# Kernel tuning notes

Hardware: AMD Instinct MI355X
Metric: run time of the kernel (lower is better)

Reference implementation:

```python
import jax, jax.numpy as jnp
import numpy as np

FM = 80            # feature_maps
N_ROUNDS = 32
NORM_EPS = 1e-3
LOSS_EPS = 1e-8


def _relu6(x):
    return jnp.clip(x, 0.0, 6.0)


def _norm(x):
    # tf.nn.moments over axis 0 + batch_normalization (no scale/offset)
    mean = jnp.mean(x, axis=0, keepdims=True)
    var = jnp.var(x, axis=0, keepdims=True)
    return (x - mean) * jax.lax.rsqrt(var + NORM_EPS)


def setup_inputs() -> dict:
    key = jax.random.key(0)
    n_vars, n_clauses, n_graphs, lits_per_clause = 100000, 420000, 100, 3
    n_cells = n_clauses * lits_per_clause
    ks = jax.random.split(key, 24)

    lit_var = jax.random.randint(ks[0], (n_cells,), 0, n_vars, dtype=jnp.int32)
    lit_neg = jax.random.randint(ks[1], (n_cells,), 0, 2, dtype=jnp.int32)
    clause_idx = jnp.repeat(jnp.arange(n_clauses, dtype=jnp.int32), lits_per_clause)
    clause_graph = jnp.repeat(jnp.arange(n_graphs, dtype=jnp.int32), n_clauses // n_graphs)

    def dense(k, fi, fo):
        return jax.random.normal(k, (fi, fo), jnp.float32) / np.sqrt(fi)

    inp = dict(
        lit_var=lit_var, lit_neg=lit_neg, clause_idx=clause_idx, clause_graph=clause_graph,
        n_vars=n_vars, n_clauses=n_clauses, n_graphs=n_graphs,
        L_init_scale=jnp.float32(1.0 / np.sqrt(FM)),
        C_init_scale=jnp.float32(1.0 / np.sqrt(FM)),
        LC_scale=jnp.float32(0.1), CL_scale=jnp.float32(0.1),
        # L_update MLP: in=3*FM (L, CL_msgs, flip(L)) -> hidden 3*FM relu6 -> FM
        Lu_W0=dense(ks[2], 3 * FM, 3 * FM), Lu_b0=jnp.zeros((3 * FM,), jnp.float32),
        Lu_W1=dense(ks[3], 3 * FM, FM),     Lu_b1=jnp.zeros((FM,), jnp.float32),
        # C_update MLP: in=2*FM (C, LC_msgs) -> hidden 2*FM relu6 -> FM
        Cu_W0=dense(ks[4], 2 * FM, 2 * FM), Cu_b0=jnp.zeros((2 * FM,), jnp.float32),
        Cu_W1=dense(ks[5], 2 * FM, FM),     Cu_b1=jnp.zeros((FM,), jnp.float32),
        # V_score MLP: in=2*FM -> 3 hidden relu6 layers of 2*FM -> 1
        Vs_W0=dense(ks[6], 2 * FM, 2 * FM), Vs_b0=jnp.zeros((2 * FM,), jnp.float32),
        Vs_W1=dense(ks[7], 2 * FM, 2 * FM), Vs_b1=jnp.zeros((2 * FM,), jnp.float32),
        Vs_W2=dense(ks[8], 2 * FM, 2 * FM), Vs_b2=jnp.zeros((2 * FM,), jnp.float32),
        Vs_W3=dense(ks[9], 2 * FM, 1),      Vs_b3=jnp.zeros((1,), jnp.float32),
    )
    return inp


def reference(lit_var, lit_neg, clause_idx, clause_graph, n_vars, n_clauses, n_graphs,
              L_init_scale, C_init_scale, LC_scale, CL_scale,
              Lu_W0, Lu_b0, Lu_W1, Lu_b1,
              Cu_W0, Cu_b0, Cu_W1, Cu_b1,
              Vs_W0, Vs_b0, Vs_W1, Vs_b1, Vs_W2, Vs_b2, Vs_W3, Vs_b3):
    n_lits = 2 * n_vars
    lit_row = lit_var + lit_neg * n_vars          # row in L for each cell
    sign = (1 - 2 * lit_neg).astype(jnp.float32)  # +1 positive literal, -1 negated

    def mlp_L(x):
        return _relu6(x @ Lu_W0 + Lu_b0) @ Lu_W1 + Lu_b1

    def mlp_C(x):
        return _relu6(x @ Cu_W0 + Cu_b0) @ Cu_W1 + Cu_b1

    def v_score(x):
        h = _relu6(x @ Vs_W0 + Vs_b0)
        h = _relu6(h @ Vs_W1 + Vs_b1)
        h = _relu6(h @ Vs_W2 + Vs_b2)
        return h @ Vs_W3 + Vs_b3

    def flip(L):
        return jnp.concatenate([L[n_vars:], L[:n_vars]], axis=0)

    def per_round_loss(logits):
        # softplus_mixed_loss over ragged clauses of signed literals
        lit_vals = logits[lit_var, 0] * sign                         # [n_cells]
        clause_sum = jax.ops.segment_sum(jax.nn.softplus(lit_vals), clause_idx,
                                         num_segments=n_clauses)     # [n_clauses]
        vc = jnp.exp(-clause_sum)
        per_clause = vc * (-jnp.log(1.0 - vc + LOSS_EPS))
        per_graph = jax.ops.segment_sum(per_clause, clause_graph, num_segments=n_graphs)
        return jnp.sum(jnp.sqrt(per_graph + 1e-6))

    L0 = jnp.ones((n_lits, FM), jnp.float32) * L_init_scale
    C0 = jnp.ones((n_clauses, FM), jnp.float32) * C_init_scale

    def round_fn(carry, _):
        L, C, loss = carry
        # CL^T @ L  (sparse gather + segment-sum over clause cells)
        LC_msgs = jax.ops.segment_sum(L[lit_row], clause_idx, num_segments=n_clauses) * LC_scale
        C = _norm(mlp_C(jnp.concatenate([C, LC_msgs], axis=-1)))
        # adj @ C  (scatter-add clause features back to literal rows)
        CL_msgs = jax.ops.segment_sum(C[clause_idx], lit_row, num_segments=n_lits) * CL_scale
        L = _norm(mlp_L(jnp.concatenate([L, CL_msgs, flip(L)], axis=-1)))
        V = jnp.concatenate([L[:n_vars], L[n_vars:]], axis=1)        # [n_vars, 2*FM]
        logits = v_score(V)
        loss = loss + per_round_loss(logits)
        return (L, C, loss), None

    (L, C, loss), _ = jax.lax.scan(round_fn, (L0, C0, jnp.float32(0.0)), None, length=N_ROUNDS)
    # final-round logits (recomputed from the final L state, identical math)
    logits = v_score(jnp.concatenate([L[:n_vars], L[n_vars:]], axis=1))
    return logits, loss / N_ROUNDS
```

## Files before the change

kernel.cpp:

```cpp
#include <hip/hip_runtime.h>
#include <hip/hip_fp8.h>
#include <math.h>


#define NROUNDS 32
#define NORM_EPS 1e-3f
#define LOSS_EPS 1e-8f

static constexpr int NV_CONST = 100000;
static constexpr int NG_CONST = 100;

typedef __attribute__((ext_vector_type(8))) short short8;
typedef __attribute__((ext_vector_type(8))) unsigned char uchar8;
typedef __attribute__((ext_vector_type(16))) unsigned char uchar16;
typedef __attribute__((ext_vector_type(4))) float f32x4;

__device__ __forceinline__ short f2bf(float f) {
    union { float f; unsigned u; } x; x.f = f;
    unsigned r = x.u + 0x7fffu + ((x.u >> 16) & 1u);
    return (short)(r >> 16);
}
__device__ __forceinline__ float bf2f(short s) {
    union { unsigned u; float f; } x; x.u = ((unsigned)(unsigned short)s) << 16;
    return x.f;
}
__device__ __forceinline__ unsigned char f2q8(float f) {
    f = fminf(fmaxf(f, -448.f), 448.f);
    __hip_fp8_e4m3 t(f);
    return t.__x;
}
__device__ __forceinline__ float q82f(unsigned char b) {
    __hip_fp8_e4m3 t; t.__x = b;
    return (float)t;
}


__global__ void k_zero_i(int* __restrict__ p, int n) {
    int i = blockIdx.x * 256 + threadIdx.x;
    if (i < n) p[i] = 0;
}
__global__ void k_fill_b(short* __restrict__ p, int n, const float* __restrict__ vp) {
    int i = blockIdx.x * 256 + threadIdx.x;
    if (i < n) p[i] = f2bf(*vp);
}
__global__ void k_fill_q8(unsigned char* __restrict__ p, int n, const float* __restrict__ vp) {
    int i = blockIdx.x * 256 + threadIdx.x;
    if (i < n) p[i] = f2q8(*vp);
}
__global__ void k_copy_int(int* __restrict__ dst, const int* __restrict__ src, int n) {
    int i = blockIdx.x * 256 + threadIdx.x;
    if (i < n) dst[i] = src[i];
}
__global__ void k_init_slabs(float* __restrict__ slabC, float* __restrict__ slabL,
                             float* __restrict__ loss_a, float nclf) {
    int i = blockIdx.x * 256 + threadIdx.x;
    if (i < 33 * 160) {
        slabC[i] = (i >= 80 && i < 160) ? nclf * (1.f - NORM_EPS) : 0.f;
        slabL[i] = 0.f;
    }
    if (i == 0) loss_a[0] = 0.f;
}

__global__ void k_litrow(const int* __restrict__ lit_var, const int* __restrict__ lit_neg,
                         int* __restrict__ litrow, int* __restrict__ lofs4,
                         int* __restrict__ counts, int ncell, int nv) {
    int i = blockIdx.x * 256 + threadIdx.x;
    if (i < ncell) {
        int r = lit_var[i] + lit_neg[i] * nv;
        litrow[i] = r;
        int cl = i / 3, t = i - cl * 3;
        lofs4[cl * 4 + t] = r * 8;
        atomicAdd(&counts[r], 1);
    }
}

__launch_bounds__(1024)
__global__ void k_scan4(const int* __restrict__ counts, int* __restrict__ row_ptr,
                        int n, int total) {
    __shared__ int sd[1024];
    __shared__ int carry;
    int tid = threadIdx.x;
    if (tid == 0) carry = 0;
    __syncthreads();
    for (int base = 0; base < n; base += 4096) {
        int i0 = base + tid * 4;
        int a0 = (i0 + 0 < n) ? counts[i0 + 0] : 0;
        int a1 = (i0 + 1 < n) ? counts[i0 + 1] : 0;
        int a2 = (i0 + 2 < n) ? counts[i0 + 2] : 0;
        int a3 = (i0 + 3 < n) ? counts[i0 + 3] : 0;
        int s = a0 + a1 + a2 + a3;
        sd[tid] = s;
        __syncthreads();
        for (int off = 1; off < 1024; off <<= 1) {
            int t = (tid >= off) ? sd[tid - off] : 0;
            __syncthreads();
            sd[tid] += t;
            __syncthreads();
        }
        int excl = carry + sd[tid] - s;
        if (i0 + 0 < n) row_ptr[i0 + 0] = excl;
        if (i0 + 1 < n) row_ptr[i0 + 1] = excl + a0;
        if (i0 + 2 < n) row_ptr[i0 + 2] = excl + a0 + a1;
        if (i0 + 3 < n) row_ptr[i0 + 3] = excl + a0 + a1 + a2;
        __syncthreads();
        if (tid == 0) carry += sd[1023];
        __syncthreads();
    }
    if (tid == 0) row_ptr[n] = total;
}

__global__ void k_fill_csr(const int* __restrict__ litrow, const int* __restrict__ clause_idx,
                           int* __restrict__ cursor, int* __restrict__ cl_of, int ncell) {
    int i = blockIdx.x * 256 + threadIdx.x;
    if (i < ncell) {
        int r = litrow[i];
        int pos = atomicAdd(&cursor[r], 1);
        cl_of[pos] = clause_idx[i];
    }
}

__global__ void k_pack_w(const float* __restrict__ W, short* __restrict__ Wp,
                         int K, int N, int KB, int NB) {
    int t = blockIdx.x * 256 + threadIdx.x;
    int tot = NB * KB * 64;
    if (t >= tot) return;
    int lane = t & 63;
    int kb = (t >> 6) % KB;
    int nb = t / (64 * KB);
    int quad = lane >> 4, l15 = lane & 15;
    int n = nb * 16 + l15;
#pragma unroll
    for (int j = 0; j < 8; ++j) {
        int k = kb * 32 + quad * 8 + j;
        float f = (k < K && n < N) ? W[(size_t)k * N + n] : 0.f;
        Wp[(size_t)t * 8 + j] = f2bf(f);
    }
}


template <int KB, int NB>
__device__ __forceinline__ void mfma_layer(const short* lds, int SK,
                                           const short8* __restrict__ Wp,
                                           f32x4* acc, int lane, int arow) {
    const int quad8 = (lane >> 4) * 8;
    short8 a[KB];
#pragma unroll
    for (int kb = 0; kb < KB; ++kb)
        a[kb] = *(const short8*)(lds + arow * SK + kb * 32 + quad8);
#pragma unroll
    for (int kb = 0; kb < KB; ++kb)
#pragma unroll
        for (int nb = 0; nb < NB; ++nb)
            acc[nb] = __builtin_amdgcn_mfma_f32_16x16x32_bf16(
                a[kb], Wp[(nb * KB + kb) * 64 + lane], acc[nb], 0, 0, 0);
}

template <int NB>
__device__ __forceinline__ void write_hidden(short* ldsH, int SKH, const f32x4* acc,
                                             const float* __restrict__ bias,
                                             int l15, int quad, int wr0) {
#pragma unroll
    for (int nb = 0; nb < NB; ++nb) {
        int c = nb * 16 + l15;
        float bv = bias[c];
#pragma unroll
        for (int reg = 0; reg < 4; ++reg) {
            int row = wr0 + quad * 4 + reg;
            float v = acc[nb][reg] + bv;
            v = fminf(fmaxf(v, 0.f), 6.f);
            ldsH[row * SKH + c] = f2bf(v);
        }
    }
}

__device__ __forceinline__ void load_stats(const float* __restrict__ slab, float Minv,
                                           float* sS, int tid) {
    if (tid < 80) {
        float m = slab[tid] * Minv;
        float v = slab[80 + tid] * Minv - m * m;
        sS[tid] = m;
        sS[80 + tid] = rsqrtf(v + NORM_EPS);
    }
}

__launch_bounds__(256, 2)
__global__ void k_c_update(short* __restrict__ Cb, unsigned char* __restrict__ Cb8,
                           const unsigned char* __restrict__ Lb8,
                           const int4* __restrict__ lofs4, const float* __restrict__ scp,
                           const short8* __restrict__ W0p, const float* __restrict__ b0,
                           const short8* __restrict__ W1p, const float* __restrict__ b1,
                           const float* __restrict__ prevSlab, float* __restrict__ nextSlab,
                           float Minv, int ncl) {
    constexpr int SK = 168;
    __shared__ short lds[64 * SK];
    __shared__ float sred[160], sC[160];
    const int lane = threadIdx.x, wy = threadIdx.y, tid = wy * 64 + lane;
    const int r0 = blockIdx.x * 64;
    const int rows = (ncl - r0 < 64) ? (ncl - r0) : 64;

    if (tid < 160) sred[tid] = 0.f;
    load_stats(prevSlab, Minv, sC, tid);
    __syncthreads();

    const float s = *scp;
    const short8* Cbv = (const short8*)Cb;
    const uchar16* Lq = (const uchar16*)Lb8;

#pragma unroll
    for (int u = 0; u < 3; ++u) {
        int it = tid + u * 256;
        int itc = (it < 640) ? it : 639;
        int lr = itc / 10, c = itc - lr * 10;
        int cl = r0 + ((lr < rows) ? lr : rows - 1);
        short8 v = Cbv[(size_t)cl * 10 + c];
        int col = c * 8;
        short8 o;
#pragma unroll
        for (int j = 0; j < 8; ++j)
            o[j] = f2bf((bf2f(v[j]) - sC[col + j]) * sC[80 + col + j]);
        if (it < 640)
            *(short8*)(lds + lr * SK + col) = o;
    }
#pragma unroll
    for (int u = 0; u < 2; ++u) {
        int it = tid + u * 256;
        int itc = (it < 320) ? it : 319;
        int lr = itc / 5, cc = itc - lr * 5;
        int cl = r0 + ((lr < rows) ? lr : rows - 1);
        int4 o4 = lofs4[cl];
        uchar16 va = Lq[(size_t)o4.x + cc];
        uchar16 vb = Lq[(size_t)o4.y + cc];
        uchar16 vc = Lq[(size_t)o4.z + cc];
        short8 o0, o1;
#pragma unroll
        for (int j = 0; j < 8; ++j) {
            o0[j] = f2bf((q82f(va[j]) + q82f(vb[j]) + q82f(vc[j])) * s);
            o1[j] = f2bf((q82f(va[8 + j]) + q82f(vb[8 + j]) + q82f(vc[8 + j])) * s);
        }
        if (it < 320) {
            *(short8*)(lds + lr * SK + 80 + cc * 16) = o0;
            *(short8*)(lds + lr * SK + 80 + cc * 16 + 8) = o1;
        }
    }
    __syncthreads();

    const int quad = lane >> 4, l15 = lane & 15, wr0 = wy * 16, arow = wr0 + l15;

    f32x4 acc[10];
#pragma unroll
    for (int nb = 0; nb < 10; ++nb) { f32x4 z = {0.f, 0.f, 0.f, 0.f}; acc[nb] = z; }
    mfma_layer<5, 10>(lds, SK, W0p, acc, lane, arow);
    write_hidden<10>(lds, SK, acc, b0, l15, quad, wr0);

    f32x4 acc2[5];
#pragma unroll
    for (int nb = 0; nb < 5; ++nb) { f32x4 z = {0.f, 0.f, 0.f, 0.f}; acc2[nb] = z; }
    mfma_layer<5, 5>(lds, SK, W1p, acc2, lane, arow);

#pragma unroll
    for (int nb = 0; nb < 5; ++nb) {
        int cc = nb * 16 + l15;
        float bv = b1[cc];
        float s1 = 0.f, s2 = 0.f;
#pragma unroll
        for (int reg = 0; reg < 4; ++reg) {
            int lr = wr0 + quad * 4 + reg;
            if (lr < rows) {
                float v = acc2[nb][reg] + bv;
                Cb[(size_t)(r0 + lr) * 80 + cc] = f2bf(v);
                Cb8[(size_t)(r0 + lr) * 128 + cc] = f2q8(v);
                s1 += v; s2 += v * v;
            }
        }
        s1 += __shfl_xor(s1, 16); s1 += __shfl_xor(s1, 32);
        s2 += __shfl_xor(s2, 16); s2 += __shfl_xor(s2, 32);
        if (quad == 0) { atomicAdd(&sred[cc], s1); atomicAdd(&sred[80 + cc], s2); }
    }
    __syncthreads();
    if (tid < 160) atomicAdd(&nextSlab[tid], sred[tid]);
}

__launch_bounds__(256)
__global__ void k_cl_gather(const unsigned char* __restrict__ Cb8,
                            const int* __restrict__ row_ptr,
                            const int* __restrict__ cl_of, const float* __restrict__ scp,
                            const float* __restrict__ slab, float Minv,
                            short* __restrict__ CLb, int nl) {
    __shared__ float sC[160];
    load_stats(slab, Minv, sC, threadIdx.x);
    __syncthreads();
    int idx = blockIdx.x * 256 + threadIdx.x;
    if (idx >= nl * 5) return;
    int r = idx / 5, c16 = idx - r * 5;
    int p0 = row_ptr[r], p1 = row_ptr[r + 1];
    float a[16];
#pragma unroll
    for (int j = 0; j < 16; ++j) a[j] = 0.f;
    const uchar16* Cq = (const uchar16*)Cb8;
    int p = p0;
    for (; p + 4 <= p1; p += 4) {
        int i0 = cl_of[p], i1 = cl_of[p + 1], i2 = cl_of[p + 2], i3 = cl_of[p + 3];
        uchar16 v0 = Cq[(size_t)i0 * 8 + c16];
        uchar16 v1 = Cq[(size_t)i1 * 8 + c16];
        uchar16 v2 = Cq[(size_t)i2 * 8 + c16];
        uchar16 v3 = Cq[(size_t)i3 * 8 + c16];
#pragma unroll
        for (int j = 0; j < 16; ++j)
            a[j] += (q82f(v0[j]) + q82f(v1[j])) + (q82f(v2[j]) + q82f(v3[j]));
    }
    for (; p < p1; ++p) {
        uchar16 v = Cq[(size_t)cl_of[p] * 8 + c16];
#pragma unroll
        for (int j = 0; j < 16; ++j) a[j] += q82f(v[j]);
    }
    float n = (float)(p1 - p0), s = *scp;
    int col = c16 * 16;
    short8 o0, o1;
#pragma unroll
    for (int j = 0; j < 8; ++j) {
        o0[j] = f2bf((a[j] - n * sC[col + j]) * sC[80 + col + j] * s);
        o1[j] = f2bf((a[8 + j] - n * sC[col + 8 + j]) * sC[80 + col + 8 + j] * s);
    }
    ((short8*)CLb)[(size_t)r * 10 + c16 * 2] = o0;
    ((short8*)CLb)[(size_t)r * 10 + c16 * 2 + 1] = o1;
}

__launch_bounds__(256, 2)
__global__ void k_l_update(short* __restrict__ Lraw, const short* __restrict__ Lb,
                           const short* __restrict__ CLb,
                           const short8* __restrict__ W0p, const float* __restrict__ b0,
                           const short8* __restrict__ W1p, const float* __restrict__ b1,
                           float* __restrict__ nextSlab, int nv) {
    constexpr int SK = 264;
    __shared__ short lds[64 * SK];
    __shared__ float sred[160];
    const int lane = threadIdx.x, wy = threadIdx.y, tid = wy * 64 + lane;
    const int vb = blockIdx.x * 32;

    if (tid < 160) sred[tid] = 0.f;
    __syncthreads();

    const short8* Lb8  = (const short8*)Lb;
    const short8* CLb8 = (const short8*)CLb;
    short8 vals[8];
#pragma unroll
    for (int u = 0; u < 8; ++u) {
        int it = tid + u * 256;
        int lr = it >> 5, c = it & 31;
        int v = (lr < 32) ? vb + lr : vb + (lr - 32);
        int half0 = (lr < 32) ? 0 : 10;
        if (c < 10) {
            vals[u] = Lb8[(size_t)v * 20 + half0 + c];
        } else if (c < 20) {
            int r = (lr < 32) ? vb + lr : vb + nv + (lr - 32);
            vals[u] = CLb8[(size_t)r * 10 + (c - 10)];
        } else if (c < 30) {
            vals[u] = Lb8[(size_t)v * 20 + (10 - half0) + (c - 20)];
        } else {
            short8 z = {0, 0, 0, 0, 0, 0, 0, 0};
            vals[u] = z;
        }
    }
#pragma unroll
    for (int u = 0; u < 8; ++u) {
        int it = tid + u * 256;
        int lr = it >> 5, c = it & 31;
        int o = (c < 10) ? c * 8 : (c < 20) ? 80 + (c - 10) * 8
              : (c < 30) ? 160 + (c - 20) * 8 : 240 + (c - 30) * 8;
        *(short8*)(lds + lr * SK + o) = vals[u];
    }
    __syncthreads();

    const int quad = lane >> 4, l15 = lane & 15, wr0 = wy * 16, arow = wr0 + l15;

    f32x4 acc[15];
#pragma unroll
    for (int nb = 0; nb < 15; ++nb) { f32x4 z = {0.f, 0.f, 0.f, 0.f}; acc[nb] = z; }
    mfma_layer<8, 15>(lds, SK, W0p, acc, lane, arow);
    write_hidden<15>(lds, SK, acc, b0, l15, quad, wr0);
    {
        int row = wr0 + (lane >> 2);
        int c = 240 + (lane & 3) * 4;
        short4 z; z.x = 0; z.y = 0; z.z = 0; z.w = 0;
        *(short4*)(lds + row * SK + c) = z;
    }

    f32x4 acc2[5];
#pragma unroll
    for (int nb = 0; nb < 5; ++nb) { f32x4 z = {0.f, 0.f, 0.f, 0.f}; acc2[nb] = z; }
    mfma_layer<8, 5>(lds, SK, W1p, acc2, lane, arow);

#pragma unroll
    for (int nb = 0; nb < 5; ++nb) {
        int cc = nb * 16 + l15;
        float bv = b1[cc];
        float s1 = 0.f, s2 = 0.f;
#pragma unroll
        for (int reg = 0; reg < 4; ++reg) {
            int lr = wr0 + quad * 4 + reg;
            int rabs = (lr < 32) ? vb + lr : vb + nv + (lr - 32);
            float v = acc2[nb][reg] + bv;
            Lraw[(size_t)rabs * 80 + cc] = f2bf(v);
            s1 += v; s2 += v * v;
        }
        s1 += __shfl_xor(s1, 16); s1 += __shfl_xor(s1, 32);
        s2 += __shfl_xor(s2, 16); s2 += __shfl_xor(s2, 32);
        if (quad == 0) { atomicAdd(&sred[cc], s1); atomicAdd(&sred[80 + cc], s2); }
    }
    __syncthreads();
    if (tid < 160) atomicAdd(&nextSlab[tid], sred[tid]);
}

__launch_bounds__(256, 2)
__global__ void k_v_head(const short* __restrict__ Lraw, const float* __restrict__ slab,
                         float Minv,
                         const short8* __restrict__ W0p, const float* __restrict__ b0,
                         const short8* __restrict__ W1p, const float* __restrict__ b1,
                         const short8* __restrict__ W2p, const float* __restrict__ b2,
                         const float* __restrict__ W3, const float* __restrict__ b3,
                         float* __restrict__ logits, short* __restrict__ Lb,
                         unsigned char* __restrict__ Lb8, int nv) {
    constexpr int SK = 168;
    __shared__ short lds[64 * SK];
    __shared__ float sW3[160], sL[160];
    const int lane = threadIdx.x, wy = threadIdx.y, tid = wy * 64 + lane;
    const int v0 = blockIdx.x * 64;
    const int cnt = (nv - v0 < 64) ? (nv - v0) : 64;

    if (tid < 160) sW3[tid] = W3[tid];
    load_stats(slab, Minv, sL, tid);
    __syncthreads();

    const short8* Lraw8 = (const short8*)Lraw;
    short8 vals[5];
#pragma unroll
    for (int u = 0; u < 5; ++u) {
        int it = tid + u * 256;
        int lr = it / 20, c = it - lr * 20;
        int v = v0 + ((lr < cnt) ? lr : cnt - 1);
        int row = (c < 10) ? v : v + nv;
        int cc = (c < 10) ? c : c - 10;
        vals[u] = Lraw8[(size_t)row * 10 + cc];
    }
#pragma unroll
    for (int u = 0; u < 5; ++u) {
        int it = tid + u * 256;
        int lr = it / 20, c = it - lr * 20;
        int v = v0 + ((lr < cnt) ? lr : cnt - 1);
        int cc = (c < 10) ? c : c - 10;
        int col = cc * 8;
        short8 o;
        uchar8 q;
#pragma unroll
        for (int j = 0; j < 8; ++j) {
            float f = (bf2f(vals[u][j]) - sL[col + j]) * sL[80 + col + j];
            o[j] = f2bf(f);
            q[j] = f2q8(f);
        }
        *(short8*)(lds + lr * SK + c * 8) = o;
        if (lr < cnt) {
            *(short8*)(Lb + (size_t)v * 160 + c * 8) = o;
            int lit = (c < 10) ? v : (v + nv);
            *(uchar8*)(Lb8 + (size_t)lit * 128 + cc * 8) = q;
        }
    }
    __syncthreads();

    const int quad = lane >> 4, l15 = lane & 15, wr0 = wy * 16, arow = wr0 + l15;

    f32x4 acc[10];
#pragma unroll
    for (int nb = 0; nb < 10; ++nb) { f32x4 z = {0.f, 0.f, 0.f, 0.f}; acc[nb] = z; }
    mfma_layer<5, 10>(lds, SK, W0p, acc, lane, arow);
    write_hidden<10>(lds, SK, acc, b0, l15, quad, wr0);

#pragma unroll
    for (int nb = 0; nb < 10; ++nb) { f32x4 z = {0.f, 0.f, 0.f, 0.f}; acc[nb] = z; }
    mfma_layer<5, 10>(lds, SK, W1p, acc, lane, arow);
    write_hidden<10>(lds, SK, acc, b1, l15, quad, wr0);

#pragma unroll
    for (int nb = 0; nb < 10; ++nb) { f32x4 z = {0.f, 0.f, 0.f, 0.f}; acc[nb] = z; }
    mfma_layer<5, 10>(lds, SK, W2p, acc, lane, arow);
    write_hidden<10>(lds, SK, acc, b2, l15, quad, wr0);
    __syncthreads();

    int lrow = tid >> 2, t4 = tid & 3;
    float v = 0.f;
    for (int c = t4; c < 160; c += 4) v += bf2f(lds[lrow * SK + c]) * sW3[c];
    v += __shfl_down(v, 2, 4);
    v += __shfl_down(v, 1, 4);
    if (t4 == 0 && lrow < cnt) logits[v0 + lrow] = v + b3[0];
}

__device__ __forceinline__ float softplusf(float x) {
    return fmaxf(x, 0.f) + log1pf(expf(-fabsf(x)));
}

__global__ void k_loss(const float* __restrict__ logits, const int* __restrict__ lit_var,
                       const int* __restrict__ lit_neg, float* __restrict__ loss_acc,
                       int cpg) {
    const int g = blockIdx.x;
    const int tid = threadIdx.x;
    float part = 0.f;
    int cend = (g + 1) * cpg;
    for (int c = g * cpg + tid; c < cend; c += 256) {
        float cs = 0.f;
#pragma unroll
        for (int t = 0; t < 3; ++t) {
            int i = c * 3 + t;
            float sign = lit_neg[i] ? -1.f : 1.f;
            cs += softplusf(logits[lit_var[i]] * sign);
        }
        float vc = expf(-cs);
        part += vc * (-log1pf(LOSS_EPS - vc));
    }
    __shared__ float red[256];
    red[tid] = part;
    __syncthreads();
    for (int s = 128; s > 0; s >>= 1) {
        if (tid < s) red[tid] += red[tid + s];
        __syncthreads();
    }
    if (tid == 0) atomicAdd(loss_acc, sqrtf(red[0] + 1e-6f));
}

__global__ void k_output(float* __restrict__ dout, const float* __restrict__ logits,
                         const float* __restrict__ loss_acc, int nv) {
    int i = blockIdx.x * 256 + threadIdx.x;
    if (i < nv) dout[i] = logits[i];
    else if (i == nv) dout[i] = loss_acc[0] * (1.f / (float)NROUNDS);
}


extern "C" void kernel_launch(void* const* d_in, const int* in_sizes, int n_in,
                              void* d_out, int out_size, void* d_ws, size_t ws_size,
                              hipStream_t stream) {
    const int* lit_var    = (const int*)d_in[0];
    const int* lit_neg    = (const int*)d_in[1];
    const int* clause_idx = (const int*)d_in[2];
    const float* Lscale = (const float*)d_in[7];
    const float* Cscale = (const float*)d_in[8];
    const float* LCs    = (const float*)d_in[9];
    const float* CLs    = (const float*)d_in[10];
    const float* LuW0 = (const float*)d_in[11]; const float* Lub0 = (const float*)d_in[12];
    const float* LuW1 = (const float*)d_in[13]; const float* Lub1 = (const float*)d_in[14];
    const float* CuW0 = (const float*)d_in[15]; const float* Cub0 = (const float*)d_in[16];
    const float* CuW1 = (const float*)d_in[17]; const float* Cub1 = (const float*)d_in[18];
    const float* VsW0 = (const float*)d_in[19]; const float* Vsb0 = (const float*)d_in[20];
    const float* VsW1 = (const float*)d_in[21]; const float* Vsb1 = (const float*)d_in[22];
    const float* VsW2 = (const float*)d_in[23]; const float* Vsb2 = (const float*)d_in[24];
    const float* VsW3 = (const float*)d_in[25]; const float* Vsb3 = (const float*)d_in[26];

    const int ncell = in_sizes[0];
    const int ncl   = in_sizes[3];
    const int nv    = NV_CONST;
    const int nl    = 2 * nv;
    const int ng    = NG_CONST;

    size_t off = 0;
    auto A = [&](size_t bytes) -> void* {
        void* q = (char*)d_ws + off;
        off = (off + bytes + 255) & ~(size_t)255;
        return q;
    };
    short* Cb    = (short*)A((size_t)ncl * 80 * 2);
    short* Lraw  = (short*)A((size_t)nl * 80 * 2);
    short* Lb    = (short*)A((size_t)nv * 160 * 2);
    short* CLb   = (short*)A((size_t)nl * 80 * 2);
    unsigned char* Lb8 = (unsigned char*)A((size_t)nl * 128);
    unsigned char* Cb8 = (unsigned char*)A((size_t)ncl * 128);
    float* logits = (float*)A((size_t)nv * 4);
    float* slabC  = (float*)A(33 * 160 * 4);
    float* slabL  = (float*)A(33 * 160 * 4);
    float* loss_a = (float*)A(256);
    int* litrow  = (int*)A((size_t)ncell * 4);
    int* lofs4   = (int*)A((size_t)ncl * 16);
    int* row_ptr = (int*)A((size_t)(nl + 1) * 4);
    int* tmp     = (int*)A((size_t)nl * 4);
    int* cl_of   = (int*)A((size_t)ncell * 4);
    short* CuW0p = (short*)A((size_t)10 * 5 * 64 * 16);
    short* CuW1p = (short*)A((size_t)5  * 5 * 64 * 16);
    short* LuW0p = (short*)A((size_t)15 * 8 * 64 * 16);
    short* LuW1p = (short*)A((size_t)5  * 8 * 64 * 16);
    short* VsW0p = (short*)A((size_t)10 * 5 * 64 * 16);
    short* VsW1p = (short*)A((size_t)10 * 5 * 64 * 16);
    short* VsW2p = (short*)A((size_t)10 * 5 * 64 * 16);

    const dim3 B64x4(64, 4, 1);

    k_zero_i<<<(nl + 255) / 256, 256, 0, stream>>>(tmp, nl);
    k_init_slabs<<<(33 * 160 + 255) / 256, 256, 0, stream>>>(slabC, slabL, loss_a, (float)ncl);
    k_litrow<<<(ncell + 255) / 256, 256, 0, stream>>>(lit_var, lit_neg, litrow, lofs4, tmp, ncell, nv);
    k_scan4<<<1, 1024, 0, stream>>>(tmp, row_ptr, nl, ncell);
    k_copy_int<<<(nl + 255) / 256, 256, 0, stream>>>(tmp, row_ptr, nl);
    k_fill_csr<<<(ncell + 255) / 256, 256, 0, stream>>>(litrow, clause_idx, tmp, cl_of, ncell);
    k_fill_b<<<(ncl * 80 + 255) / 256, 256, 0, stream>>>(Cb, ncl * 80, Cscale);
    k_fill_b<<<(nl * 80 + 255) / 256, 256, 0, stream>>>(Lraw, nl * 80, Lscale);
    k_fill_b<<<(nv * 160 + 255) / 256, 256, 0, stream>>>(Lb, nv * 160, Lscale);
    k_fill_q8<<<(nl * 128 + 255) / 256, 256, 0, stream>>>(Lb8, nl * 128, Lscale);
    k_fill_q8<<<(ncl * 128 + 255) / 256, 256, 0, stream>>>(Cb8, ncl * 128, Cscale);
    k_pack_w<<<(10 * 5 * 64 + 255) / 256, 256, 0, stream>>>(CuW0, CuW0p, 160, 160, 5, 10);
    k_pack_w<<<(5  * 5 * 64 + 255) / 256, 256, 0, stream>>>(CuW1, CuW1p, 160, 80, 5, 5);
    k_pack_w<<<(15 * 8 * 64 + 255) / 256, 256, 0, stream>>>(LuW0, LuW0p, 240, 240, 8, 15);
    k_pack_w<<<(5  * 8 * 64 + 255) / 256, 256, 0, stream>>>(LuW1, LuW1p, 240, 80, 8, 5);
    k_pack_w<<<(10 * 5 * 64 + 255) / 256, 256, 0, stream>>>(VsW0, VsW0p, 160, 160, 5, 10);
    k_pack_w<<<(10 * 5 * 64 + 255) / 256, 256, 0, stream>>>(VsW1, VsW1p, 160, 160, 5, 10);
    k_pack_w<<<(10 * 5 * 64 + 255) / 256, 256, 0, stream>>>(VsW2, VsW2p, 160, 160, 5, 10);

    const int cblk  = (ncl + 63) / 64;
    const int lblk  = nv / 32;
    const int vblk  = (nv + 63) / 64;
    const int clblk = (nl * 5 + 255) / 256;
    const float MinvC = 1.f / (float)ncl;
    const float MinvL = 1.f / (float)nl;

    for (int r = 0; r < NROUNDS; ++r) {
        float* sCr  = slabC + (size_t)r * 160;
        float* sCr1 = slabC + (size_t)(r + 1) * 160;
        float* sLr1 = slabL + (size_t)(r + 1) * 160;
        k_c_update<<<cblk, B64x4, 0, stream>>>(
            Cb, Cb8, Lb8, (const int4*)lofs4, LCs, (const short8*)CuW0p, Cub0,
            (const short8*)CuW1p, Cub1, sCr, sCr1, MinvC, ncl);
        k_cl_gather<<<clblk, 256, 0, stream>>>(Cb8, row_ptr, cl_of, CLs, sCr1, MinvC, CLb, nl);
        k_l_update<<<lblk, B64x4, 0, stream>>>(
            Lraw, Lb, CLb, (const short8*)LuW0p, Lub0, (const short8*)LuW1p, Lub1, sLr1, nv);
        k_v_head<<<vblk, B64x4, 0, stream>>>(
            Lraw, sLr1, MinvL, (const short8*)VsW0p, Vsb0, (const short8*)VsW1p, Vsb1,
            (const short8*)VsW2p, Vsb2, VsW3, Vsb3, logits, Lb, Lb8, nv);
        k_loss<<<ng, 256, 0, stream>>>(logits, lit_var, lit_neg, loss_a, ncl / ng);
    }

    k_output<<<(nv + 1 + 255) / 256, 256, 0, stream>>>((float*)d_out, logits, loss_a, nv);
}
```

Baseline: 15.69 ms.

## Drop normalized L buffer and normalize raw L on the fly in L update

Removes the separate normalized bf16 L buffer that the V-head wrote each round. The L-update kernel now reads the raw pre-norm L rows and applies the previous round's mean/rstd stats while staging them into LDS. To support round 0, the L stats slab is initialized like the C slab. The loss kernel reads one packed var/neg-sign array instead of two index arrays, and the C-update uses nontemporal loads and stores for the bf16 C buffer. This trades one full-size write and read of L per round for some extra ALU work on loads.

Result: no change. 15.54 ms (-0.9%).

```diff
diff --git a/kernel.cpp b/kernel.cpp
--- a/kernel.cpp
+++ b/kernel.cpp
@@ -52,24 +52,27 @@
     if (i < n) dst[i] = src[i];
 }
 __global__ void k_init_slabs(float* __restrict__ slabC, float* __restrict__ slabL,
-                             float* __restrict__ loss_a, float nclf) {
+                             float* __restrict__ loss_a, float nclf, float nlf) {
     int i = blockIdx.x * 256 + threadIdx.x;
     if (i < 33 * 160) {
         slabC[i] = (i >= 80 && i < 160) ? nclf * (1.f - NORM_EPS) : 0.f;
-        slabL[i] = 0.f;
+        slabL[i] = (i >= 80 && i < 160) ? nlf * (1.f - NORM_EPS) : 0.f;
     }
     if (i == 0) loss_a[0] = 0.f;
 }
 
 __global__ void k_litrow(const int* __restrict__ lit_var, const int* __restrict__ lit_neg,
                          int* __restrict__ litrow, int* __restrict__ lofs4,
+                         int* __restrict__ cellpk,
                          int* __restrict__ counts, int ncell, int nv) {
     int i = blockIdx.x * 256 + threadIdx.x;
     if (i < ncell) {
-        int r = lit_var[i] + lit_neg[i] * nv;
+        int vv = lit_var[i], ng = lit_neg[i];
+        int r = vv + ng * nv;
         litrow[i] = r;
         int cl = i / 3, t = i - cl * 3;
         lofs4[cl * 4 + t] = r * 8;
+        cellpk[i] = vv | (ng << 31);
         atomicAdd(&counts[r], 1);
     }
 }
@@ -212,7 +215,7 @@
         int itc = (it < 640) ? it : 639;
         int lr = itc / 10, c = itc - lr * 10;
         int cl = r0 + ((lr < rows) ? lr : rows - 1);
-        short8 v = Cbv[(size_t)cl * 10 + c];
+        short8 v = __builtin_nontemporal_load(&Cbv[(size_t)cl * 10 + c]);
         int col = c * 8;
         short8 o;
 #pragma unroll
@@ -267,7 +270,7 @@
             int lr = wr0 + quad * 4 + reg;
             if (lr < rows) {
                 float v = acc2[nb][reg] + bv;
-                Cb[(size_t)(r0 + lr) * 80 + cc] = f2bf(v);
+                __builtin_nontemporal_store(f2bf(v), &Cb[(size_t)(r0 + lr) * 80 + cc]);
                 Cb8[(size_t)(r0 + lr) * 128 + cc] = f2q8(v);
                 s1 += v; s2 += v * v;
             }
@@ -326,36 +329,36 @@
 }
 
 __launch_bounds__(256, 2)
-__global__ void k_l_update(short* __restrict__ Lraw, const short* __restrict__ Lb,
-                           const short* __restrict__ CLb,
+__global__ void k_l_update(short* __restrict__ Lraw, const short* __restrict__ CLb,
                            const short8* __restrict__ W0p, const float* __restrict__ b0,
                            const short8* __restrict__ W1p, const float* __restrict__ b1,
-                           float* __restrict__ nextSlab, int nv) {
+                           const float* __restrict__ prevSlab, float* __restrict__ nextSlab,
+                           float Minv, int nv) {
     constexpr int SK = 264;
     __shared__ short lds[64 * SK];
-    __shared__ float sred[160];
+    __shared__ float sred[160], sL[160];
     const int lane = threadIdx.x, wy = threadIdx.y, tid = wy * 64 + lane;
     const int vb = blockIdx.x * 32;
 
     if (tid < 160) sred[tid] = 0.f;
-    __syncthreads();
-
-    const short8* Lb8  = (const short8*)Lb;
+    load_stats(prevSlab, Minv, sL, tid);
+    __syncthreads();
+
+    const short8* Lr8  = (const short8*)Lraw;
     const short8* CLb8 = (const short8*)CLb;
     short8 vals[8];
 #pragma unroll
     for (int u = 0; u < 8; ++u) {
         int it = tid + u * 256;
         int lr = it >> 5, c = it & 31;
-        int v = (lr < 32) ? vb + lr : vb + (lr - 32);
-        int half0 = (lr < 32) ? 0 : 10;
+        int own = (lr < 32) ? vb + lr : vb + nv + (lr - 32);
+        int opp = (lr < 32) ? vb + nv + lr : vb + (lr - 32);
         if (c < 10) {
-            vals[u] = Lb8[(size_t)v * 20 + half0 + c];
+            vals[u] = Lr8[(size_t)own * 10 + c];
         } else if (c < 20) {
-            int r = (lr < 32) ? vb + lr : vb + nv + (lr - 32);
-            vals[u] = CLb8[(size_t)r * 10 + (c - 10)];
+            vals[u] = CLb8[(size_t)own * 10 + (c - 10)];
         } else if (c < 30) {
-            vals[u] = Lb8[(size_t)v * 20 + (10 - half0) + (c - 20)];
+            vals[u] = Lr8[(size_t)opp * 10 + (c - 20)];
         } else {
             short8 z = {0, 0, 0, 0, 0, 0, 0, 0};
             vals[u] = z;
@@ -365,9 +368,16 @@
     for (int u = 0; u < 8; ++u) {
         int it = tid + u * 256;
         int lr = it >> 5, c = it & 31;
+        short8 w = vals[u];
+        if (c < 10 || (c >= 20 && c < 30)) {
+            int base = (c < 10) ? c * 8 : (c - 20) * 8;
+#pragma unroll
+            for (int j = 0; j < 8; ++j)
+                w[j] = f2bf((bf2f(w[j]) - sL[base + j]) * sL[80 + base + j]);
+        }
         int o = (c < 10) ? c * 8 : (c < 20) ? 80 + (c - 10) * 8
               : (c < 30) ? 160 + (c - 20) * 8 : 240 + (c - 30) * 8;
-        *(short8*)(lds + lr * SK + o) = vals[u];
+        *(short8*)(lds + lr * SK + o) = w;
     }
     __syncthreads();
 
@@ -418,7 +428,7 @@
                          const short8* __restrict__ W1p, const float* __restrict__ b1,
                          const short8* __restrict__ W2p, const float* __restrict__ b2,
                          const float* __restrict__ W3, const float* __restrict__ b3,
-                         float* __restrict__ logits, short* __restrict__ Lb,
+                         float* __restrict__ logits,
                          unsigned char* __restrict__ Lb8, int nv) {
     constexpr int SK = 168;
     __shared__ short lds[64 * SK];
@@ -459,7 +469,6 @@
         }
         *(short8*)(lds + lr * SK + c * 8) = o;
         if (lr < cnt) {
-            *(short8*)(Lb + (size_t)v * 160 + c * 8) = o;
             int lit = (c < 10) ? v : (v + nv);
             *(uchar8*)(Lb8 + (size_t)lit * 128 + cc * 8) = q;
         }
@@ -497,9 +506,8 @@
     return fmaxf(x, 0.f) + log1pf(expf(-fabsf(x)));
 }
 
-__global__ void k_loss(const float* __restrict__ logits, const int* __restrict__ lit_var,
-                       const int* __restrict__ lit_neg, float* __restrict__ loss_acc,
-                       int cpg) {
+__global__ void k_loss(const float* __restrict__ logits, const int* __restrict__ cellpk,
+                       float* __restrict__ loss_acc, int cpg) {
     const int g = blockIdx.x;
     const int tid = threadIdx.x;
     float part = 0.f;
@@ -508,9 +516,9 @@
         float cs = 0.f;
 #pragma unroll
         for (int t = 0; t < 3; ++t) {
-            int i = c * 3 + t;
-            float sign = lit_neg[i] ? -1.f : 1.f;
-            cs += softplusf(logits[lit_var[i]] * sign);
+            int cp = cellpk[c * 3 + t];
+            float sign = (cp < 0) ? -1.f : 1.f;
+            cs += softplusf(logits[cp & 0x7fffffff] * sign);
         }
         float vc = expf(-cs);
         part += vc * (-log1pf(LOSS_EPS - vc));
@@ -566,7 +574,6 @@
     };
     short* Cb    = (short*)A((size_t)ncl * 80 * 2);
     short* Lraw  = (short*)A((size_t)nl * 80 * 2);
-    short* Lb    = (short*)A((size_t)nv * 160 * 2);
     short* CLb   = (short*)A((size_t)nl * 80 * 2);
     unsigned char* Lb8 = (unsigned char*)A((size_t)nl * 128);
     unsigned char* Cb8 = (unsigned char*)A((size_t)ncl * 128);
@@ -576,6 +583,7 @@
     float* loss_a = (float*)A(256);
     int* litrow  = (int*)A((size_t)ncell * 4);
     int* lofs4   = (int*)A((size_t)ncl * 16);
+    int* cellpk  = (int*)A((size_t)ncell * 4);
     int* row_ptr = (int*)A((size_t)(nl + 1) * 4);
     int* tmp     = (int*)A((size_t)nl * 4);
     int* cl_of   = (int*)A((size_t)ncell * 4);
@@ -590,14 +598,15 @@
     const dim3 B64x4(64, 4, 1);
 
     k_zero_i<<<(nl + 255) / 256, 256, 0, stream>>>(tmp, nl);
-    k_init_slabs<<<(33 * 160 + 255) / 256, 256, 0, stream>>>(slabC, slabL, loss_a, (float)ncl);
-    k_litrow<<<(ncell + 255) / 256, 256, 0, stream>>>(lit_var, lit_neg, litrow, lofs4, tmp, ncell, nv);
+    k_init_slabs<<<(33 * 160 + 255) / 256, 256, 0, stream>>>(slabC, slabL, loss_a,
+                                                             (float)ncl, (float)nl);
+    k_litrow<<<(ncell + 255) / 256, 256, 0, stream>>>(lit_var, lit_neg, litrow, lofs4,
+                                                      cellpk, tmp, ncell, nv);
     k_scan4<<<1, 1024, 0, stream>>>(tmp, row_ptr, nl, ncell);
     k_copy_int<<<(nl + 255) / 256, 256, 0, stream>>>(tmp, row_ptr, nl);
     k_fill_csr<<<(ncell + 255) / 256, 256, 0, stream>>>(litrow, clause_idx, tmp, cl_of, ncell);
     k_fill_b<<<(ncl * 80 + 255) / 256, 256, 0, stream>>>(Cb, ncl * 80, Cscale);
     k_fill_b<<<(nl * 80 + 255) / 256, 256, 0, stream>>>(Lraw, nl * 80, Lscale);
-    k_fill_b<<<(nv * 160 + 255) / 256, 256, 0, stream>>>(Lb, nv * 160, Lscale);
     k_fill_q8<<<(nl * 128 + 255) / 256, 256, 0, stream>>>(Lb8, nl * 128, Lscale);
     k_fill_q8<<<(ncl * 128 + 255) / 256, 256, 0, stream>>>(Cb8, ncl * 128, Cscale);
     k_pack_w<<<(10 * 5 * 64 + 255) / 256, 256, 0, stream>>>(CuW0, CuW0p, 160, 160, 5, 10);
@@ -618,17 +627,19 @@
     for (int r = 0; r < NROUNDS; ++r) {
         float* sCr  = slabC + (size_t)r * 160;
         float* sCr1 = slabC + (size_t)(r + 1) * 160;
+        float* sLr  = slabL + (size_t)r * 160;
         float* sLr1 = slabL + (size_t)(r + 1) * 160;
         k_c_update<<<cblk, B64x4, 0, stream>>>(
             Cb, Cb8, Lb8, (const int4*)lofs4, LCs, (const short8*)CuW0p, Cub0,
             (const short8*)CuW1p, Cub1, sCr, sCr1, MinvC, ncl);
         k_cl_gather<<<clblk, 256, 0, stream>>>(Cb8, row_ptr, cl_of, CLs, sCr1, MinvC, CLb, nl);
         k_l_update<<<lblk, B64x4, 0, stream>>>(
-            Lraw, Lb, CLb, (const short8*)LuW0p, Lub0, (const short8*)LuW1p, Lub1, sLr1, nv);
+            Lraw, CLb, (const short8*)LuW0p, Lub0, (const short8*)LuW1p, Lub1,
+            sLr, sLr1, MinvL, nv);
         k_v_head<<<vblk, B64x4, 0, stream>>>(
             Lraw, sLr1, MinvL, (const short8*)VsW0p, Vsb0, (const short8*)VsW1p, Vsb1,
-            (const short8*)VsW2p, Vsb2, VsW3, Vsb3, logits, Lb, Lb8, nv);
-        k_loss<<<ng, 256, 0, stream>>>(logits, lit_var, lit_neg, loss_a, ncl / ng);
+            (const short8*)VsW2p, Vsb2, VsW3, Vsb3, logits, Lb8, nv);
+        k_loss<<<ng, 256, 0, stream>>>(logits, cellpk, loss_a, ncl / ng);
     }
 
     k_output<<<(nv + 1 + 255) / 256, 256, 0, stream>>>((float*)d_out, logits, loss_a, nv);
```
